# Optimization experiments

Measured on AMD Instinct MI355X. Metric: run time of the kernel, lower is better.

Reference implementation:

```python
import jax, jax.numpy as jnp
import numpy as np

C = 512  # n_channels

def _maxpool2x2(t):
    # t: [B, C, H, W] -> [B, C, H//2, W//2]
    B, Cc, H, W = t.shape
    return t.reshape(B, Cc, H // 2, 2, W // 2, 2).max(axis=(3, 5))

def setup_inputs() -> dict:
    key = jax.random.key(0)
    ks = jax.random.split(key, 6)
    B, H, W = 16, 64, 64
    x = jax.random.normal(ks[0], (B, C, H, W), dtype=jnp.float32)
    # 1x1 conv weights (spectral-normalized convs, no bias) stored as [out, in]
    wq = jax.random.normal(ks[1], (C // 8, C), dtype=jnp.float32) * 0.05
    wk = jax.random.normal(ks[2], (C // 8, C), dtype=jnp.float32) * 0.05
    wv = jax.random.normal(ks[3], (C // 2, C), dtype=jnp.float32) * 0.05
    wo = jax.random.normal(ks[4], (C, C // 2), dtype=jnp.float32) * 0.05
    gamma = jnp.zeros((1,), dtype=jnp.float32) + 0.5  # nonzero so output depends on attention path
    return {"x": x, "wq": wq, "wk": wk, "wv": wv, "wo": wo, "gamma": gamma}

def reference(x, wq, wk, wv, wo, gamma):
    B, Cc, H, W = x.shape
    n = H * W
    # 1x1 convs are channel-mixing matmuls
    f = jnp.einsum('oc,bchw->bohw', wq, x).reshape(B, Cc // 8, n)            # [B, C/8, n]
    g = _maxpool2x2(jnp.einsum('oc,bchw->bohw', wk, x)).reshape(B, Cc // 8, n // 4)  # [B, C/8, n/4]
    h = _maxpool2x2(jnp.einsum('oc,bchw->bohw', wv, x)).reshape(B, Cc // 2, n // 4)  # [B, C/2, n/4]
    # attention: softmax over pooled kv positions
    beta = jax.nn.softmax(jnp.einsum('bcn,bcm->bnm', f, g), axis=-1)         # [B, n, n/4]
    o = jnp.einsum('bcm,bnm->bcn', h, beta).reshape(B, Cc // 2, H, W)        # [B, C/2, H, W]
    o = jnp.einsum('oc,bchw->bohw', wo, o)                                   # [B, C, H, W]
    return gamma.reshape(()) * o + x
```

## Files before the change

### kernel.cpp

```cpp
#include <hip/hip_runtime.h>
#include <cstdint>
#include <cstddef>

namespace {

constexpr int kB  = 16;
constexpr int kC  = 512;
constexpr int kCQ = 64;
constexpr int kCV = 256;
constexpr int kN  = 4096;
constexpr int kM  = 1024;

typedef _Float16 f16;
typedef _Float16 f16x8 __attribute__((ext_vector_type(8)));
typedef float    f32x4 __attribute__((ext_vector_type(4)));

__global__ __launch_bounds__(256)
void convert_weights_kernel(const float* __restrict__ wq,
                            const float* __restrict__ wk,
                            const float* __restrict__ wv,
                            const float* __restrict__ wo,
                            const float* __restrict__ gamma,
                            f16* __restrict__ wcat,
                            f16* __restrict__ woh)
{
    const int idx = blockIdx.x * 256 + threadIdx.x;
    if (idx < 49152) {
        const int e = idx * 4;
        const int r = e >> 9, c = e & 511;
        const float* src = (r < 64)  ? (wq + ((size_t)r << 9))
                         : (r < 128) ? (wk + ((size_t)(r - 64) << 9))
                                     : (wv + ((size_t)(r - 128) << 9));
        float4 v = *(const float4*)(src + c);
        union { f16 h4[4]; uint2 u; } pk;
        pk.h4[0] = (f16)v.x; pk.h4[1] = (f16)v.y;
        pk.h4[2] = (f16)v.z; pk.h4[3] = (f16)v.w;
        *(uint2*)(wcat + e) = pk.u;
    } else {
        const int e = (idx - 49152) * 4;
        const float g = gamma[0];
        float4 v = *(const float4*)(wo + e);
        union { f16 h4[4]; uint2 u; } pk;
        pk.h4[0] = (f16)(g * v.x); pk.h4[1] = (f16)(g * v.y);
        pk.h4[2] = (f16)(g * v.z); pk.h4[3] = (f16)(g * v.w);
        *(uint2*)(woh + e) = pk.u;
    }
}

__global__ __launch_bounds__(512, 4)
void proj_pool_mfma(const float* __restrict__ x,
                    const f16* __restrict__ wcat,
                    f16* __restrict__ fT,
                    f16* __restrict__ gT,
                    f16* __restrict__ h)
{
    const int nt  = blockIdx.x;
    const int mt  = blockIdx.y;
    const int b   = blockIdx.z;
    const int tid = threadIdx.x;
    const int w    = tid >> 6;
    const int lane = tid & 63;
    const int quad = lane >> 4;
    const int lq   = lane & 15;
    const int wr   = w >> 1;
    const int wc   = w & 1;

    __shared__ alignas(16) f16 Bs[2][128 * 36];

    const f16*   Ab = wcat + (size_t)mt * 192 * kC;
    const float* Xb = x + (size_t)b * kC * kN + nt * 128;

    f32x4 acc[3][4];
#pragma unroll
    for (int i = 0; i < 3; ++i)
#pragma unroll
        for (int j = 0; j < 4; ++j) acc[i][j] = {0.f, 0.f, 0.f, 0.f};

    const int bn = tid & 127;
    const int kg = tid >> 7;
    float xv[8];

    auto loadB = [&](int k0) {
#pragma unroll
        for (int j = 0; j < 8; ++j) xv[j] = Xb[(size_t)(k0 + kg * 8 + j) * kN + bn];
    };
    auto writeB = [&](int buf) {
        union { f16 hh[8]; uint4 u; } pk;
#pragma unroll
        for (int j = 0; j < 8; ++j) pk.hh[j] = (f16)xv[j];
        *(uint4*)&Bs[buf][bn * 36 + kg * 8] = pk.u;
    };

    const f16* arow[3];
#pragma unroll
    for (int ti = 0; ti < 3; ++ti)
        arow[ti] = Ab + (size_t)(wr * 48 + ti * 16 + lq) * kC + quad * 8;

    f16x8 afp[3];
#pragma unroll
    for (int ti = 0; ti < 3; ++ti) afp[ti] = *(const f16x8*)(arow[ti]);

    loadB(0);
    writeB(0);
    __syncthreads();

    for (int ks = 0; ks < 16; ++ks) {
        const int cur = ks & 1;
        if (ks < 15) loadB((ks + 1) * 32);

        f16x8 afc[3];
#pragma unroll
        for (int ti = 0; ti < 3; ++ti) afc[ti] = afp[ti];
        if (ks < 15) {
#pragma unroll
            for (int ti = 0; ti < 3; ++ti)
                afp[ti] = *(const f16x8*)(arow[ti] + (ks + 1) * 32);
        }

        f16x8 bsv[4];
#pragma unroll
        for (int tj = 0; tj < 4; ++tj) {
            const int col = (tj < 2) ? (wc * 32 + tj * 16 + lq)
                                     : (64 + wc * 32 + (tj - 2) * 16 + lq);
            bsv[tj] = *(const f16x8*)&Bs[cur][col * 36 + quad * 8];
        }
        __builtin_amdgcn_s_setprio(1);
#pragma unroll
        for (int ti = 0; ti < 3; ++ti)
#pragma unroll
            for (int tj = 0; tj < 4; ++tj)
                acc[ti][tj] = __builtin_amdgcn_mfma_f32_16x16x32_f16(
                    afc[ti], bsv[tj], acc[ti][tj], 0, 0, 0);
        __builtin_amdgcn_s_setprio(0);

        if (ks < 15) writeB(cur ^ 1);
        __syncthreads();
    }

#pragma unroll
    for (int ti = 0; ti < 3; ++ti) {
        const int ch0 = mt * 192 + wr * 48 + ti * 16;
        if (ch0 < 64) {
            f16* fb = fT + (size_t)b * kN * kCQ;
#pragma unroll
            for (int tj = 0; tj < 4; ++tj) {
                const int col = (tj < 2) ? (wc * 32 + tj * 16 + lq)
                                         : (64 + wc * 32 + (tj - 2) * 16 + lq);
                const int n = nt * 128 + col;
                union { f16 h4[4]; uint2 u; } pk;
#pragma unroll
                for (int r = 0; r < 4; ++r) pk.h4[r] = (f16)acc[ti][tj][r];
                *(uint2*)(fb + (size_t)n * kCQ + ch0 + quad * 4) = pk.u;
            }
        } else {
#pragma unroll
            for (int tjp = 0; tjp < 2; ++tjp) {
                float p[4];
#pragma unroll
                for (int r = 0; r < 4; ++r) {
                    float v = fmaxf(acc[ti][tjp][r], acc[ti][tjp + 2][r]);
                    v = fmaxf(v, __shfl_xor(v, 1, 64));
                    p[r] = v;
                }
                const int m = nt * 32 + wc * 16 + tjp * 8 + (lq >> 1);
                if ((lq & 1) == 0) {
                    if (ch0 < 128) {
                        union { f16 h4[4]; uint2 u; } pk;
#pragma unroll
                        for (int r = 0; r < 4; ++r) pk.h4[r] = (f16)p[r];
                        *(uint2*)(gT + ((size_t)b * kM + m) * kCQ + (ch0 - 64) + quad * 4) = pk.u;
                    } else {
#pragma unroll
                        for (int r = 0; r < 4; ++r) {
                            const int ch = ch0 - 128 + quad * 4 + r;
                            h[((size_t)b * kCV + ch) * kM + m] = (f16)p[r];
                        }
                    }
                }
            }
        }
    }
}

__global__ __launch_bounds__(256, 2)
void attn_out_kernel(const f16* __restrict__ fT,
                     const f16* __restrict__ gT,
                     const f16* __restrict__ hmat,
                     const f16* __restrict__ woh,
                     const float* __restrict__ x,
                     float* __restrict__ out)
{
    const int qt   = blockIdx.x;
    const int b    = blockIdx.y;
    const int tid  = threadIdx.x;
    const int w    = tid >> 6;
    const int lane = tid & 63;
    const int quad = lane >> 4;
    const int lq   = lane & 15;

    __shared__ union alignas(16) SMem {
        struct {
            f16 fsT[128 * 72];
            f16 gsT[2][32 * 64];
            f16 hs[2][256 * 40];
            f16 ps[64 * 40];
        } p1;
        struct {
            f16 osT[64 * 264];
            f16 wos[2][256 * 40];
        } p2;
    } sm;

    {
        const f16* fb = fT + ((size_t)b * kN + qt * 128) * kCQ;
#pragma unroll
        for (int p = 0; p < 4; ++p) {
            const int unit = tid + p * 256;
            const int q = unit >> 3, u = unit & 7;
            *(uint4*)&sm.p1.fsT[q * 72 + u * 8] = *(const uint4*)(fb + q * 64 + u * 8);
        }
    }
    __syncthreads();

    const f16x8 afA0 = *(const f16x8*)&sm.p1.fsT[(w * 16 + lq) * 72 + quad * 8];
    const f16x8 afA1 = *(const f16x8*)&sm.p1.fsT[(w * 16 + lq) * 72 + 32 + quad * 8];
    const f16x8 afB0 = *(const f16x8*)&sm.p1.fsT[(64 + w * 16 + lq) * 72 + quad * 8];
    const f16x8 afB1 = *(const f16x8*)&sm.p1.fsT[(64 + w * 16 + lq) * 72 + 32 + quad * 8];

    float mA = -3.0e38f, lA = 0.f, mB = -3.0e38f, lB = 0.f;
    f32x4 o_accA[16], o_accB[16];
#pragma unroll
    for (int ci = 0; ci < 16; ++ci) {
        o_accA[ci] = {0.f, 0.f, 0.f, 0.f};
        o_accB[ci] = {0.f, 0.f, 0.f, 0.f};
    }

    const f16* gTb = gT + (size_t)b * kM * kCQ;
    const f16* hb  = hmat + (size_t)b * kCV * kM;

    const int gm = tid >> 3, gsu = tid & 7, ggu = gsu ^ (gm & 7);
    const int hc = tid >> 2, hu = tid & 3;
    uint4 pg, ph[4];
    auto load_chunk = [&](int m0) {
        pg = *(const uint4*)(gTb + (size_t)(m0 + gm) * kCQ + ggu * 8);
#pragma unroll
        for (int p = 0; p < 4; ++p)
            ph[p] = *(const uint4*)(hb + (size_t)(hc + p * 64) * kM + m0 + hu * 8);
    };
    auto write_chunk = [&](int buf) {
        *(uint4*)&sm.p1.gsT[buf][gm * 64 + gsu * 8] = pg;
#pragma unroll
        for (int p = 0; p < 4; ++p)
            *(uint4*)&sm.p1.hs[buf][(hc + p * 64) * 40 + hu * 8] = ph[p];
    };

    load_chunk(0);
    write_chunk(0);
    load_chunk(32);
    __syncthreads();

    for (int mi = 0; mi < 32; ++mi) {
        const int cur = mi & 1;
        if (mi < 31) write_chunk(cur ^ 1);
        if (mi < 30) load_chunk((mi + 2) * 32);

        const int mr0 = lq, mr1 = 16 + lq;
        const f16* gsc = &sm.p1.gsT[cur][0];
        const f16x8 bg00 = *(const f16x8*)&gsc[mr0 * 64 + ((quad       ^ (mr0 & 7)) * 8)];
        const f16x8 bg01 = *(const f16x8*)&gsc[mr0 * 64 + (((4 + quad) ^ (mr0 & 7)) * 8)];
        const f16x8 bg10 = *(const f16x8*)&gsc[mr1 * 64 + ((quad       ^ (mr1 & 7)) * 8)];
        const f16x8 bg11 = *(const f16x8*)&gsc[mr1 * 64 + (((4 + quad) ^ (mr1 & 7)) * 8)];
        f32x4 s0A = {0.f,0.f,0.f,0.f}, s1A = {0.f,0.f,0.f,0.f};
        f32x4 s0B = {0.f,0.f,0.f,0.f}, s1B = {0.f,0.f,0.f,0.f};
        s0A = __builtin_amdgcn_mfma_f32_16x16x32_f16(bg00, afA0, s0A, 0, 0, 0);
        s0A = __builtin_amdgcn_mfma_f32_16x16x32_f16(bg01, afA1, s0A, 0, 0, 0);
        s1A = __builtin_amdgcn_mfma_f32_16x16x32_f16(bg10, afA0, s1A, 0, 0, 0);
        s1A = __builtin_amdgcn_mfma_f32_16x16x32_f16(bg11, afA1, s1A, 0, 0, 0);
        s0B = __builtin_amdgcn_mfma_f32_16x16x32_f16(bg00, afB0, s0B, 0, 0, 0);
        s0B = __builtin_amdgcn_mfma_f32_16x16x32_f16(bg01, afB1, s0B, 0, 0, 0);
        s1B = __builtin_amdgcn_mfma_f32_16x16x32_f16(bg10, afB0, s1B, 0, 0, 0);
        s1B = __builtin_amdgcn_mfma_f32_16x16x32_f16(bg11, afB1, s1B, 0, 0, 0);

        float alA;
        {
            float cm = fmaxf(fmaxf(fmaxf(s0A[0], s0A[1]), fmaxf(s0A[2], s0A[3])),
                             fmaxf(fmaxf(s1A[0], s1A[1]), fmaxf(s1A[2], s1A[3])));
            cm = fmaxf(cm, __shfl_xor(cm, 16, 64));
            cm = fmaxf(cm, __shfl_xor(cm, 32, 64));
            const float nm = fmaxf(mA, cm);
            alA = __expf(mA - nm);
            float e0[4], e1[4];
#pragma unroll
            for (int r = 0; r < 4; ++r) { e0[r] = __expf(s0A[r] - nm); e1[r] = __expf(s1A[r] - nm); }
            float psum = (e0[0]+e0[1])+(e0[2]+e0[3])+(e1[0]+e1[1])+(e1[2]+e1[3]);
            psum += __shfl_xor(psum, 16, 64);
            psum += __shfl_xor(psum, 32, 64);
            mA = nm;
            lA = lA * alA + psum;
            union { f16 h4[4]; uint2 u; } pk0, pk1;
#pragma unroll
            for (int r = 0; r < 4; ++r) { pk0.h4[r] = (f16)e0[r]; pk1.h4[r] = (f16)e1[r]; }
            *(uint2*)&sm.p1.ps[(w * 16 + lq) * 40 + quad * 4]      = pk0.u;
            *(uint2*)&sm.p1.ps[(w * 16 + lq) * 40 + 16 + quad * 4] = pk1.u;
        }
        const f16x8 bpA = *(const f16x8*)&sm.p1.ps[(w * 16 + lq) * 40 + quad * 8];
        __builtin_amdgcn_sched_barrier(0);

        float alB;
        {
            float cm = fmaxf(fmaxf(fmaxf(s0B[0], s0B[1]), fmaxf(s0B[2], s0B[3])),
                             fmaxf(fmaxf(s1B[0], s1B[1]), fmaxf(s1B[2], s1B[3])));
            cm = fmaxf(cm, __shfl_xor(cm, 16, 64));
            cm = fmaxf(cm, __shfl_xor(cm, 32, 64));
            const float nm = fmaxf(mB, cm);
            alB = __expf(mB - nm);
            float e0[4], e1[4];
#pragma unroll
            for (int r = 0; r < 4; ++r) { e0[r] = __expf(s0B[r] - nm); e1[r] = __expf(s1B[r] - nm); }
            float psum = (e0[0]+e0[1])+(e0[2]+e0[3])+(e1[0]+e1[1])+(e1[2]+e1[3]);
            psum += __shfl_xor(psum, 16, 64);
            psum += __shfl_xor(psum, 32, 64);
            mB = nm;
            lB = lB * alB + psum;
            union { f16 h4[4]; uint2 u; } pk0, pk1;
#pragma unroll
            for (int r = 0; r < 4; ++r) { pk0.h4[r] = (f16)e0[r]; pk1.h4[r] = (f16)e1[r]; }
            *(uint2*)&sm.p1.ps[(w * 16 + lq) * 40 + quad * 4]      = pk0.u;
            *(uint2*)&sm.p1.ps[(w * 16 + lq) * 40 + 16 + quad * 4] = pk1.u;
        }
        const f16x8 bpB = *(const f16x8*)&sm.p1.ps[(w * 16 + lq) * 40 + quad * 8];
        __builtin_amdgcn_sched_barrier(0);

        __builtin_amdgcn_s_setprio(1);
#pragma unroll
        for (int ci = 0; ci < 16; ++ci) {
            const f16x8 ha = *(const f16x8*)&sm.p1.hs[cur][(ci * 16 + lq) * 40 + quad * 8];
            o_accA[ci] *= alA;
            o_accA[ci] = __builtin_amdgcn_mfma_f32_16x16x32_f16(ha, bpA, o_accA[ci], 0, 0, 0);
            o_accB[ci] *= alB;
            o_accB[ci] = __builtin_amdgcn_mfma_f32_16x16x32_f16(ha, bpB, o_accB[ci], 0, 0, 0);
        }
        __builtin_amdgcn_s_setprio(0);

        __syncthreads();
    }

    const float invA = 1.0f / lA;
    const float invB = 1.0f / lB;

#pragma unroll
    for (int ci = 0; ci < 16; ++ci) {
        union { f16 h4[4]; uint2 u; } pk;
#pragma unroll
        for (int r = 0; r < 4; ++r) pk.h4[r] = (f16)(o_accA[ci][r] * invA);
        *(uint2*)&sm.p2.osT[(w * 16 + lq) * 264 + ci * 16 + quad * 4] = pk.u;
    }

    const int woc = tid >> 2, wu = tid & 3;
    uint4 pw[4];
    auto load_w = [&](int sp) {
#pragma unroll
        for (int p = 0; p < 4; ++p)
            pw[p] = *(const uint4*)(woh +
                (size_t)((sp >> 3) * 256 + woc + p * 64) * 256 + (sp & 7) * 32 + wu * 8);
    };
    auto write_w = [&](int buf) {
#pragma unroll
        for (int p = 0; p < 4; ++p)
            *(uint4*)&sm.p2.wos[buf][(woc + p * 64) * 40 + wu * 8] = pw[p];
    };

    load_w(0);
    write_w(0);
    load_w(1);
    __syncthreads();

    for (int tile = 0; tile < 2; ++tile) {
        for (int half = 0; half < 2; ++half) {
            f32x4 acc2[16];
#pragma unroll
            for (int os = 0; os < 16; ++os) acc2[os] = {0.f, 0.f, 0.f, 0.f};

            for (int ck = 0; ck < 8; ++ck) {
                const int sidx = tile * 16 + half * 8 + ck;
                const int cur2 = sidx & 1;
                if (sidx < 31) write_w(cur2 ^ 1);
                if (sidx < 30) load_w((sidx + 2) & 15);

                const f16x8 bo = *(const f16x8*)&sm.p2.osT[(w * 16 + lq) * 264 + ck * 32 + quad * 8];
                __builtin_amdgcn_s_setprio(1);
#pragma unroll
                for (int os = 0; os < 16; ++os) {
                    const f16x8 wa = *(const f16x8*)&sm.p2.wos[cur2][(os * 16 + lq) * 40 + quad * 8];
                    acc2[os] = __builtin_amdgcn_mfma_f32_16x16x32_f16(wa, bo, acc2[os], 0, 0, 0);
                }
                __builtin_amdgcn_s_setprio(0);
                __syncthreads();
            }

            const int n0 = qt * 128 + tile * 64 + w * 16 + lq;
#pragma unroll
            for (int os = 0; os < 16; ++os) {
#pragma unroll
                for (int r = 0; r < 4; ++r) {
                    const int oc = half * 256 + os * 16 + quad * 4 + r;
                    const size_t idx = ((size_t)b * kC + oc) * (size_t)kN + n0;
                    out[idx] = acc2[os][r] + x[idx];
                }
            }
        }
        if (tile == 0) {
#pragma unroll
            for (int ci = 0; ci < 16; ++ci) {
                union { f16 h4[4]; uint2 u; } pk;
#pragma unroll
                for (int r = 0; r < 4; ++r) pk.h4[r] = (f16)(o_accB[ci][r] * invB);
                *(uint2*)&sm.p2.osT[(w * 16 + lq) * 264 + ci * 16 + quad * 4] = pk.u;
            }
        }
    }
}

}

extern "C" void kernel_launch(void* const* d_in, const int* in_sizes, int n_in,
                              void* d_out, int out_size, void* d_ws, size_t ws_size,
                              hipStream_t stream) {
    const float* x     = (const float*)d_in[0];
    const float* wq    = (const float*)d_in[1];
    const float* wk    = (const float*)d_in[2];
    const float* wv    = (const float*)d_in[3];
    const float* wo    = (const float*)d_in[4];
    const float* gamma = (const float*)d_in[5];
    float* out = (float*)d_out;

    f16* fT   = (f16*)d_ws;
    f16* gT   = fT  + (size_t)kB * kN * kCQ;
    f16* hw   = gT  + (size_t)kB * kM * kCQ;
    f16* woh  = hw  + (size_t)kB * kCV * kM;
    f16* wcat = woh + (size_t)kC * kCV;

    hipLaunchKernelGGL(convert_weights_kernel, dim3(320), dim3(256), 0, stream,
                       wq, wk, wv, wo, gamma, wcat, woh);
    hipLaunchKernelGGL(proj_pool_mfma, dim3(32, 2, kB), dim3(512), 0, stream,
                       x, wcat, fT, gT, hw);
    hipLaunchKernelGGL(attn_out_kernel, dim3(32, kB), dim3(256), 0, stream,
                       fT, gT, hw, woh, x, out);
}
```

Baseline: 437.4 us.

## Deepen conv prefetch, lazy softmax rescale, remap blocks, raise occupancy

The projection kernel now prefetches x three K-steps ahead in registers and fully unrolls its K loop. The attention kernel loads its query fragments straight from global memory, dropping the fsT shared buffer. It also skips the online-softmax max update and accumulator rescale unless the block max grows by more than 8, and reorders block indices across batches. The output-projection weight buffer goes from double to single buffered with an extra barrier, which frees shared memory for launch bounds that target 3 blocks per SM. The risks are register spills under the tighter bound, lost load/compute overlap from the single buffer, and a small fp16 overflow margin from the lazy rescale.

```diff
diff --git a/kernel.cpp b/kernel.cpp
--- a/kernel.cpp
+++ b/kernel.cpp
@@ -78,18 +78,7 @@
 
     const int bn = tid & 127;
     const int kg = tid >> 7;
-    float xv[8];
-
-    auto loadB = [&](int k0) {
-#pragma unroll
-        for (int j = 0; j < 8; ++j) xv[j] = Xb[(size_t)(k0 + kg * 8 + j) * kN + bn];
-    };
-    auto writeB = [&](int buf) {
-        union { f16 hh[8]; uint4 u; } pk;
-#pragma unroll
-        for (int j = 0; j < 8; ++j) pk.hh[j] = (f16)xv[j];
-        *(uint4*)&Bs[buf][bn * 36 + kg * 8] = pk.u;
-    };
+    float xv[3][8];
 
     const f16* arow[3];
 #pragma unroll
@@ -100,21 +89,35 @@
 #pragma unroll
     for (int ti = 0; ti < 3; ++ti) afp[ti] = *(const f16x8*)(arow[ti]);
 
-    loadB(0);
-    writeB(0);
+#pragma unroll
+    for (int j = 0; j < 8; ++j) xv[0][j] = Xb[(size_t)(kg * 8 + j) * kN + bn];
+    {
+        union { f16 hh[8]; uint4 u; } pk;
+#pragma unroll
+        for (int j = 0; j < 8; ++j) pk.hh[j] = (f16)xv[0][j];
+        *(uint4*)&Bs[0][bn * 36 + kg * 8] = pk.u;
+    }
+#pragma unroll
+    for (int j = 0; j < 8; ++j) xv[1][j] = Xb[(size_t)(32 + kg * 8 + j) * kN + bn];
+#pragma unroll
+    for (int j = 0; j < 8; ++j) xv[2][j] = Xb[(size_t)(64 + kg * 8 + j) * kN + bn];
     __syncthreads();
 
-    for (int ks = 0; ks < 16; ++ks) {
-        const int cur = ks & 1;
-        if (ks < 15) loadB((ks + 1) * 32);
-
+#pragma unroll
+    for (int t = 0; t < 16; ++t) {
+        const int buf = t & 1;
+        if (t + 3 < 16) {
+#pragma unroll
+            for (int j = 0; j < 8; ++j)
+                xv[t % 3][j] = Xb[(size_t)((t + 3) * 32 + kg * 8 + j) * kN + bn];
+        }
         f16x8 afc[3];
 #pragma unroll
         for (int ti = 0; ti < 3; ++ti) afc[ti] = afp[ti];
-        if (ks < 15) {
+        if (t < 15) {
 #pragma unroll
             for (int ti = 0; ti < 3; ++ti)
-                afp[ti] = *(const f16x8*)(arow[ti] + (ks + 1) * 32);
+                afp[ti] = *(const f16x8*)(arow[ti] + (t + 1) * 32);
         }
 
         f16x8 bsv[4];
@@ -122,7 +125,7 @@
         for (int tj = 0; tj < 4; ++tj) {
             const int col = (tj < 2) ? (wc * 32 + tj * 16 + lq)
                                      : (64 + wc * 32 + (tj - 2) * 16 + lq);
-            bsv[tj] = *(const f16x8*)&Bs[cur][col * 36 + quad * 8];
+            bsv[tj] = *(const f16x8*)&Bs[buf][col * 36 + quad * 8];
         }
         __builtin_amdgcn_s_setprio(1);
 #pragma unroll
@@ -133,7 +136,12 @@
                     afc[ti], bsv[tj], acc[ti][tj], 0, 0, 0);
         __builtin_amdgcn_s_setprio(0);
 
-        if (ks < 15) writeB(cur ^ 1);
+        if (t < 15) {
+            union { f16 hh[8]; uint4 u; } pk;
+#pragma unroll
+            for (int j = 0; j < 8; ++j) pk.hh[j] = (f16)xv[(t + 1) % 3][j];
+            *(uint4*)&Bs[buf ^ 1][bn * 36 + kg * 8] = pk.u;
+        }
         __syncthreads();
     }
 
@@ -182,7 +190,7 @@
     }
 }
 
-__global__ __launch_bounds__(256, 2)
+__global__ __launch_bounds__(256, 3)
 void attn_out_kernel(const f16* __restrict__ fT,
                      const f16* __restrict__ gT,
                      const f16* __restrict__ hmat,
@@ -190,8 +198,10 @@
                      const float* __restrict__ x,
                      float* __restrict__ out)
 {
-    const int qt   = blockIdx.x;
-    const int b    = blockIdx.y;
+    const int s   = blockIdx.y * 32 + blockIdx.x;
+    const int wid = (s & 7) * 64 + (s >> 3);
+    const int qt  = wid & 31;
+    const int b   = wid >> 5;
     const int tid  = threadIdx.x;
     const int w    = tid >> 6;
     const int lane = tid & 63;
@@ -200,32 +210,21 @@
 
     __shared__ union alignas(16) SMem {
         struct {
-            f16 fsT[128 * 72];
             f16 gsT[2][32 * 64];
             f16 hs[2][256 * 40];
             f16 ps[64 * 40];
         } p1;
         struct {
             f16 osT[64 * 264];
-            f16 wos[2][256 * 40];
+            f16 wos[256 * 40];
         } p2;
     } sm;
 
-    {
-        const f16* fb = fT + ((size_t)b * kN + qt * 128) * kCQ;
-#pragma unroll
-        for (int p = 0; p < 4; ++p) {
-            const int unit = tid + p * 256;
-            const int q = unit >> 3, u = unit & 7;
-            *(uint4*)&sm.p1.fsT[q * 72 + u * 8] = *(const uint4*)(fb + q * 64 + u * 8);
-        }
-    }
-    __syncthreads();
-
-    const f16x8 afA0 = *(const f16x8*)&sm.p1.fsT[(w * 16 + lq) * 72 + quad * 8];
-    const f16x8 afA1 = *(const f16x8*)&sm.p1.fsT[(w * 16 + lq) * 72 + 32 + quad * 8];
-    const f16x8 afB0 = *(const f16x8*)&sm.p1.fsT[(64 + w * 16 + lq) * 72 + quad * 8];
-    const f16x8 afB1 = *(const f16x8*)&sm.p1.fsT[(64 + w * 16 + lq) * 72 + 32 + quad * 8];
+    const f16* fqA = fT + ((size_t)b * kN + qt * 128 + w * 16 + lq) * kCQ;
+    const f16x8 afA0 = *(const f16x8*)(fqA + quad * 8);
+    const f16x8 afA1 = *(const f16x8*)(fqA + 32 + quad * 8);
+    const f16x8 afB0 = *(const f16x8*)(fqA + 64 * kCQ + quad * 8);
+    const f16x8 afB1 = *(const f16x8*)(fqA + 64 * kCQ + 32 + quad * 8);
 
     float mA = -3.0e38f, lA = 0.f, mB = -3.0e38f, lB = 0.f;
     f32x4 o_accA[16], o_accB[16];
@@ -281,21 +280,24 @@
         s1B = __builtin_amdgcn_mfma_f32_16x16x32_f16(bg10, afB0, s1B, 0, 0, 0);
         s1B = __builtin_amdgcn_mfma_f32_16x16x32_f16(bg11, afB1, s1B, 0, 0, 0);
 
-        float alA;
+        float alA = 1.f; bool needA;
         {
             float cm = fmaxf(fmaxf(fmaxf(s0A[0], s0A[1]), fmaxf(s0A[2], s0A[3])),
                              fmaxf(fmaxf(s1A[0], s1A[1]), fmaxf(s1A[2], s1A[3])));
             cm = fmaxf(cm, __shfl_xor(cm, 16, 64));
             cm = fmaxf(cm, __shfl_xor(cm, 32, 64));
-            const float nm = fmaxf(mA, cm);
-            alA = __expf(mA - nm);
+            needA = !__all(cm - mA <= 8.f);
+            if (needA) {
+                const float nm = fmaxf(mA, cm);
+                alA = __expf(mA - nm);
+                mA = nm;
+            }
             float e0[4], e1[4];
 #pragma unroll
-            for (int r = 0; r < 4; ++r) { e0[r] = __expf(s0A[r] - nm); e1[r] = __expf(s1A[r] - nm); }
+            for (int r = 0; r < 4; ++r) { e0[r] = __expf(s0A[r] - mA); e1[r] = __expf(s1A[r] - mA); }
             float psum = (e0[0]+e0[1])+(e0[2]+e0[3])+(e1[0]+e1[1])+(e1[2]+e1[3]);
             psum += __shfl_xor(psum, 16, 64);
             psum += __shfl_xor(psum, 32, 64);
-            mA = nm;
             lA = lA * alA + psum;
             union { f16 h4[4]; uint2 u; } pk0, pk1;
 #pragma unroll
@@ -306,21 +308,24 @@
         const f16x8 bpA = *(const f16x8*)&sm.p1.ps[(w * 16 + lq) * 40 + quad * 8];
         __builtin_amdgcn_sched_barrier(0);
 
-        float alB;
+        float alB = 1.f; bool needB;
         {
             float cm = fmaxf(fmaxf(fmaxf(s0B[0], s0B[1]), fmaxf(s0B[2], s0B[3])),
                              fmaxf(fmaxf(s1B[0], s1B[1]), fmaxf(s1B[2], s1B[3])));
             cm = fmaxf(cm, __shfl_xor(cm, 16, 64));
             cm = fmaxf(cm, __shfl_xor(cm, 32, 64));
-            const float nm = fmaxf(mB, cm);
-            alB = __expf(mB - nm);
+            needB = !__all(cm - mB <= 8.f);
+            if (needB) {
+                const float nm = fmaxf(mB, cm);
+                alB = __expf(mB - nm);
+                mB = nm;
+            }
             float e0[4], e1[4];
 #pragma unroll
-            for (int r = 0; r < 4; ++r) { e0[r] = __expf(s0B[r] - nm); e1[r] = __expf(s1B[r] - nm); }
+            for (int r = 0; r < 4; ++r) { e0[r] = __expf(s0B[r] - mB); e1[r] = __expf(s1B[r] - mB); }
             float psum = (e0[0]+e0[1])+(e0[2]+e0[3])+(e1[0]+e1[1])+(e1[2]+e1[3]);
             psum += __shfl_xor(psum, 16, 64);
             psum += __shfl_xor(psum, 32, 64);
-            mB = nm;
             lB = lB * alB + psum;
             union { f16 h4[4]; uint2 u; } pk0, pk1;
 #pragma unroll
@@ -331,13 +336,20 @@
         const f16x8 bpB = *(const f16x8*)&sm.p1.ps[(w * 16 + lq) * 40 + quad * 8];
         __builtin_amdgcn_sched_barrier(0);
 
+        if (needA) {
+#pragma unroll
+            for (int ci = 0; ci < 16; ++ci) o_accA[ci] *= alA;
+        }
+        if (needB) {
+#pragma unroll
+            for (int ci = 0; ci < 16; ++ci) o_accB[ci] *= alB;
+        }
+
         __builtin_amdgcn_s_setprio(1);
 #pragma unroll
         for (int ci = 0; ci < 16; ++ci) {
             const f16x8 ha = *(const f16x8*)&sm.p1.hs[cur][(ci * 16 + lq) * 40 + quad * 8];
-            o_accA[ci] *= alA;
             o_accA[ci] = __builtin_amdgcn_mfma_f32_16x16x32_f16(ha, bpA, o_accA[ci], 0, 0, 0);
-            o_accB[ci] *= alB;
             o_accB[ci] = __builtin_amdgcn_mfma_f32_16x16x32_f16(ha, bpB, o_accB[ci], 0, 0, 0);
         }
         __builtin_amdgcn_s_setprio(0);
@@ -364,14 +376,14 @@
             pw[p] = *(const uint4*)(woh +
                 (size_t)((sp >> 3) * 256 + woc + p * 64) * 256 + (sp & 7) * 32 + wu * 8);
     };
-    auto write_w = [&](int buf) {
+    auto write_w = [&]() {
 #pragma unroll
         for (int p = 0; p < 4; ++p)
-            *(uint4*)&sm.p2.wos[buf][(woc + p * 64) * 40 + wu * 8] = pw[p];
+            *(uint4*)&sm.p2.wos[(woc + p * 64) * 40 + wu * 8] = pw[p];
     };
 
     load_w(0);
-    write_w(0);
+    write_w();
     load_w(1);
     __syncthreads();
 
@@ -382,19 +394,20 @@
             for (int os = 0; os < 16; ++os) acc2[os] = {0.f, 0.f, 0.f, 0.f};
 
             for (int ck = 0; ck < 8; ++ck) {
-                const int sidx = tile * 16 + half * 8 + ck;
-                const int cur2 = sidx & 1;
-                if (sidx < 31) write_w(cur2 ^ 1);
-                if (sidx < 30) load_w((sidx + 2) & 15);
-
+                const int g = tile * 16 + half * 8 + ck;
                 const f16x8 bo = *(const f16x8*)&sm.p2.osT[(w * 16 + lq) * 264 + ck * 32 + quad * 8];
                 __builtin_amdgcn_s_setprio(1);
 #pragma unroll
                 for (int os = 0; os < 16; ++os) {
-                    const f16x8 wa = *(const f16x8*)&sm.p2.wos[cur2][(os * 16 + lq) * 40 + quad * 8];
+                    const f16x8 wa = *(const f16x8*)&sm.p2.wos[(os * 16 + lq) * 40 + quad * 8];
                     acc2[os] = __builtin_amdgcn_mfma_f32_16x16x32_f16(wa, bo, acc2[os], 0, 0, 0);
                 }
                 __builtin_amdgcn_s_setprio(0);
+                __syncthreads();
+                if (g < 31) {
+                    write_w();
+                    load_w((g + 2) & 15);
+                }
                 __syncthreads();
             }
 
```

Measured after the change: 724.2 us. 1.66x slower.
